# Kernel tuning notes

Measured on AMD Instinct MI355X. Metric: run time of the kernel, lower is better.

Reference implementation:

```python
import jax, jax.numpy as jnp
import numpy as np

V, D, DK, H, HID, NB = 8192, 768, 64, 12, 3072, 4
B, S = 4, 1024


def setup_inputs() -> dict:
    key = jax.random.key(0)
    ks = jax.random.split(key, 10)
    def n(k, shape):
        return jax.random.normal(k, shape, jnp.float32) * 0.02
    return dict(
        X=jax.random.uniform(ks[0], (B, S, V), jnp.float32),
        emb_w=n(ks[1], (V, D)), emb_b=jnp.zeros((D,), jnp.float32),
        Wq=n(ks[2], (NB, H, D, DK)), bq=jnp.zeros((NB, H, DK), jnp.float32),
        Wk=n(ks[3], (NB, H, D, DK)), bk=jnp.zeros((NB, H, DK), jnp.float32),
        Wv=n(ks[4], (NB, H, D, DK)), bv=jnp.zeros((NB, H, DK), jnp.float32),
        Wo=n(ks[5], (NB, H * DK, D)), bo=jnp.zeros((NB, D), jnp.float32),
        W1=n(ks[6], (NB, D, HID)), b1=jnp.zeros((NB, HID), jnp.float32),
        W2=n(ks[7], (NB, HID, D)), b2=jnp.zeros((NB, D), jnp.float32),
        Wout=n(ks[8], (D, V)), bout=jnp.zeros((V,), jnp.float32),
    )


def layernorm(X):
    # custom LayerNorm: no eps, no affine, population variance over dim 2
    mu = jnp.mean(X, axis=2, keepdims=True)
    sigma = jnp.sqrt(jnp.mean(jnp.square(X - mu), axis=2, keepdims=True))
    return (X - mu) / sigma


def reference(X, emb_w, emb_b, Wq, bq, Wk, bk, Wv, bv, Wo, bo, W1, b1, W2, b2, Wout, bout):
    b, s, _ = X.shape
    sqrt_dk = jnp.sqrt(jnp.float32(DK))
    causal = jnp.tril(jnp.ones((s, s), bool))  # tril applied to scores BEFORE softmax (zeros, not -inf) — faithful
    X = X @ emb_w + emb_b  # [b,s,d]
    for i in range(NB):
        Q = jnp.einsum('bsd,hde->bhse', X, Wq[i]) + bq[i][None, :, None, :]
        K = jnp.einsum('bsd,hde->bhse', X, Wk[i]) + bk[i][None, :, None, :]
        Vv = jnp.einsum('bsd,hde->bhse', X, Wv[i]) + bv[i][None, :, None, :]
        scores = jnp.einsum('bhqe,bhke->bhqk', Q, K)
        scores = jnp.where(causal, scores, 0.0) / sqrt_dk
        A = jax.nn.softmax(scores, axis=-1)
        # original einsum 'ijk,ijl->ijl': sum attention weights over k, scale V
        head_out = jnp.sum(A, axis=-1, keepdims=True) * Vv  # [b,h,s,dk]
        cat = head_out.transpose(0, 2, 1, 3).reshape(b, s, H * DK)
        O = cat @ Wo[i] + bo[i]
        X = layernorm(X + O)
        F = jax.nn.relu(X @ W1[i] + b1[i]) @ W2[i] + b2[i]
        X = layernorm(X + F)
    return jax.nn.softmax(X @ Wout + bout, axis=2)
```

## Files before the change

### kernel.cpp

```cpp
#include <hip/hip_runtime.h>

typedef __bf16 bf16_t;
typedef __bf16 bf16x8 __attribute__((ext_vector_type(8)));
typedef float f32x4 __attribute__((ext_vector_type(4)));

#define BM 128
#define BN 128
#define BK 32
#define LDK 40

__device__ inline uint4 pack_bf16x8(float4 a, float4 b)
{
    union { bf16_t h[8]; uint4 u; } cv;
    cv.h[0] = (bf16_t)a.x; cv.h[1] = (bf16_t)a.y;
    cv.h[2] = (bf16_t)a.z; cv.h[3] = (bf16_t)a.w;
    cv.h[4] = (bf16_t)b.x; cv.h[5] = (bf16_t)b.y;
    cv.h[6] = (bf16_t)b.z; cv.h[7] = (bf16_t)b.w;
    return cv.u;
}

template<bool AF32>
__global__ __launch_bounds__(256, 2)
void gemm_bf16(const bf16_t* __restrict__ A, const float* __restrict__ Af,
               const bf16_t* __restrict__ Bt, const float* __restrict__ bias,
               float* __restrict__ Cf, bf16_t* __restrict__ Cbf,
               int M, int N, int K, int relu, int kChunk, long zStride)
{
    __shared__ bf16_t As[BM * LDK];
    __shared__ bf16_t Bs[BN * LDK];

    const int tid  = threadIdx.x;
    const int m0   = blockIdx.y * BM;
    const int n0   = blockIdx.x * BN;
    const int z    = blockIdx.z;
    const int wave = tid >> 6;
    const int lane = tid & 63;
    const int wm   = (wave & 1) * 64;
    const int wn   = (wave >> 1) * 64;
    const int lr   = lane & 15;
    const int lq   = lane >> 4;

    int kBeg = 0, kEnd = K;
    const float* biasP = bias;
    if (kChunk > 0) {
        kBeg = z * kChunk;
        kEnd = min(K, kBeg + kChunk);
        Cf  += (long)z * M * N;
        if (z != 0) biasP = nullptr;
    } else if (zStride != 0) {
        if constexpr (AF32) Af += (long)z * zStride;
        else                A  += (long)z * zStride;
        Bt += (long)z * zStride;
        if (Cf)  Cf  += (long)z * zStride;
        if (Cbf) Cbf += (long)z * zStride;
    }

    f32x4 acc[4][4];
#pragma unroll
    for (int i = 0; i < 4; i++)
#pragma unroll
        for (int j = 0; j < 4; j++) acc[i][j] = (f32x4){0.f, 0.f, 0.f, 0.f};

    const int c0 = tid, c1 = tid + 256;
    const int ar0 = c0 >> 2, ak0 = (c0 & 3) * 8;
    const int ar1 = c1 >> 2, ak1 = (c1 & 3) * 8;

    const bf16_t* Bptr = Bt + (long)n0 * K;

    for (int k0 = kBeg; k0 < kEnd; k0 += BK) {
        uint4 av0, av1;
        if constexpr (AF32) {
            const float* p0 = Af + (long)(m0 + ar0) * K + k0 + ak0;
            const float* p1 = Af + (long)(m0 + ar1) * K + k0 + ak1;
            float4 a00 = *(const float4*)p0, a01 = *(const float4*)(p0 + 4);
            float4 a10 = *(const float4*)p1, a11 = *(const float4*)(p1 + 4);
            av0 = pack_bf16x8(a00, a01);
            av1 = pack_bf16x8(a10, a11);
        } else {
            av0 = *(const uint4*)(A + (long)(m0 + ar0) * K + k0 + ak0);
            av1 = *(const uint4*)(A + (long)(m0 + ar1) * K + k0 + ak1);
        }
        uint4 bv0 = *(const uint4*)(Bptr + (long)ar0 * K + k0 + ak0);
        uint4 bv1 = *(const uint4*)(Bptr + (long)ar1 * K + k0 + ak1);
        __syncthreads();
        *(uint4*)&As[ar0 * LDK + ak0] = av0;
        *(uint4*)&As[ar1 * LDK + ak1] = av1;
        *(uint4*)&Bs[ar0 * LDK + ak0] = bv0;
        *(uint4*)&Bs[ar1 * LDK + ak1] = bv1;
        __syncthreads();

        bf16x8 af[4], bfr[4];
#pragma unroll
        for (int i = 0; i < 4; i++) {
            af[i]  = *(bf16x8*)&As[(wm + i * 16 + lr) * LDK + lq * 8];
            bfr[i] = *(bf16x8*)&Bs[(wn + i * 16 + lr) * LDK + lq * 8];
        }
#pragma unroll
        for (int i = 0; i < 4; i++)
#pragma unroll
            for (int j = 0; j < 4; j++)
                acc[i][j] = __builtin_amdgcn_mfma_f32_16x16x32_bf16(
                    af[i], bfr[j], acc[i][j], 0, 0, 0);
    }

#pragma unroll
    for (int i = 0; i < 4; i++) {
#pragma unroll
        for (int j = 0; j < 4; j++) {
            const int col = n0 + wn + j * 16 + lr;
            const float bval = biasP ? biasP[col] : 0.f;
#pragma unroll
            for (int r = 0; r < 4; r++) {
                const int row = m0 + wm + i * 16 + lq * 4 + r;
                float v = acc[i][j][r] + bval;
                if (relu) v = fmaxf(v, 0.f);
                const long idx = (long)row * N + col;
                if (Cf)  Cf[idx] = v;
                if (Cbf) Cbf[idx] = (bf16_t)v;
            }
        }
    }
}

__global__ void transpose_cast(const float* __restrict__ in, bf16_t* __restrict__ out,
                               int R, int C, long inStrideZ, long outStrideZ)
{
    __shared__ float t[32][33];
    const float* inz = in + inStrideZ * blockIdx.z;
    bf16_t* outz = out + outStrideZ * blockIdx.z;
    const int c0 = blockIdx.x * 32;
    const int r0 = blockIdx.y * 32;
    const int tx = threadIdx.x, ty = threadIdx.y;
#pragma unroll
    for (int dy = 0; dy < 32; dy += 8)
        t[ty + dy][tx] = inz[(long)(r0 + ty + dy) * C + c0 + tx];
    __syncthreads();
#pragma unroll
    for (int dy = 0; dy < 32; dy += 8)
        outz[(long)(c0 + ty + dy) * R + r0 + tx] = (bf16_t)t[tx][ty + dy];
}

__global__ void build_wvn(const float* __restrict__ Wv, bf16_t* __restrict__ WvN)
{
    const long o = (long)blockIdx.x * 256 + threadIdx.x;
    const int e = (int)(o & 63);
    const int h = (int)((o >> 6) % 12);
    const long t = o / 768;
    const int d = (int)(t % 768);
    const int i = (int)(t / 768);
    WvN[o] = (bf16_t)Wv[(((long)(i * 12 + h) * 768 + d) << 6) + e];
}

__global__ __launch_bounds__(256)
void build_bvo(const float* __restrict__ Wo, const float* __restrict__ bv,
               const float* __restrict__ bo, float* __restrict__ bvo)
{
    const int i = blockIdx.y;
    const int j = blockIdx.x * 256 + threadIdx.x;
    const float* w = Wo + (long)i * 589824 + j;
    const float* b = bv + i * 768;
    float s = bo[i * 768 + j];
    for (int n = 0; n < 768; n++) s += b[n] * w[(long)n * 768];
    bvo[i * 768 + j] = s;
}

__global__ __launch_bounds__(256)
void reduce_cast(const float* __restrict__ P, long pStride, int nP,
                 float* __restrict__ outF, bf16_t* __restrict__ outBf, long n)
{
    const long i = ((long)blockIdx.x * 256 + threadIdx.x) * 4;
    if (i >= n) return;
    float4 s = *(const float4*)(P + i);
    for (int p = 1; p < nP; p++) {
        float4 t = *(const float4*)(P + (long)p * pStride + i);
        s.x += t.x; s.y += t.y; s.z += t.z; s.w += t.w;
    }
    *(float4*)(outF + i) = s;
    union { bf16_t h[4]; uint2 u; } cv;
    cv.h[0] = (bf16_t)s.x; cv.h[1] = (bf16_t)s.y;
    cv.h[2] = (bf16_t)s.z; cv.h[3] = (bf16_t)s.w;
    *(uint2*)(outBf + i) = cv.u;
}

__global__ __launch_bounds__(256)
void ln_residual(float* __restrict__ X, const float* __restrict__ P,
                 long pStride, int nP, bf16_t* __restrict__ Xbf)
{
    __shared__ float red[8];
    const long base = (long)blockIdx.x * 768;
    const int tid = threadIdx.x;
    float s[3];
#pragma unroll
    for (int j = 0; j < 3; j++) {
        const int idx = tid + j * 256;
        float v = X[base + idx];
        for (int p = 0; p < nP; p++) v += P[(long)p * pStride + base + idx];
        s[j] = v;
    }
    float sum = s[0] + s[1] + s[2];
    for (int o = 32; o > 0; o >>= 1) sum += __shfl_down(sum, o, 64);
    if ((tid & 63) == 0) red[tid >> 6] = sum;
    __syncthreads();
    const float mu = (red[0] + red[1] + red[2] + red[3]) * (1.0f / 768.0f);
    float d0 = s[0] - mu, d1 = s[1] - mu, d2 = s[2] - mu;
    float sq = d0 * d0 + d1 * d1 + d2 * d2;
    for (int o = 32; o > 0; o >>= 1) sq += __shfl_down(sq, o, 64);
    if ((tid & 63) == 0) red[4 + (tid >> 6)] = sq;
    __syncthreads();
    const float var = (red[4] + red[5] + red[6] + red[7]) * (1.0f / 768.0f);
    const float rstd = 1.0f / sqrtf(var);
#pragma unroll
    for (int j = 0; j < 3; j++) {
        const int idx = tid + j * 256;
        const float v = (s[j] - mu) * rstd;
        X[base + idx] = v;
        Xbf[base + idx] = (bf16_t)v;
    }
}

__global__ __launch_bounds__(256)
void softmax_inplace(float* __restrict__ P)
{
    __shared__ float red[8];
    const long base = (long)blockIdx.x * 8192;
    const int tid = threadIdx.x;
    float v[32];
    float mx = -1e30f;
#pragma unroll
    for (int j = 0; j < 32; j++) {
        v[j] = P[base + tid + j * 256];
        mx = fmaxf(mx, v[j]);
    }
    for (int o = 32; o > 0; o >>= 1) mx = fmaxf(mx, __shfl_down(mx, o, 64));
    if ((tid & 63) == 0) red[tid >> 6] = mx;
    __syncthreads();
    mx = fmaxf(fmaxf(red[0], red[1]), fmaxf(red[2], red[3]));
    float sum = 0.f;
#pragma unroll
    for (int j = 0; j < 32; j++) {
        v[j] = __expf(v[j] - mx);
        sum += v[j];
    }
    for (int o = 32; o > 0; o >>= 1) sum += __shfl_down(sum, o, 64);
    if ((tid & 63) == 0) red[4 + (tid >> 6)] = sum;
    __syncthreads();
    const float inv = 1.0f / (red[4] + red[5] + red[6] + red[7]);
#pragma unroll
    for (int j = 0; j < 32; j++) P[base + tid + j * 256] = v[j] * inv;
}

extern "C" void kernel_launch(void* const* d_in, const int* in_sizes, int n_in,
                              void* d_out, int out_size, void* d_ws, size_t ws_size,
                              hipStream_t stream)
{
    (void)in_sizes; (void)n_in; (void)out_size; (void)ws_size;
    const float* X0   = (const float*)d_in[0];
    const float* embw = (const float*)d_in[1];
    const float* embb = (const float*)d_in[2];
    const float* Wv   = (const float*)d_in[7];
    const float* bv   = (const float*)d_in[8];
    const float* Wo   = (const float*)d_in[9];
    const float* bo   = (const float*)d_in[10];
    const float* W1   = (const float*)d_in[11];
    const float* b1   = (const float*)d_in[12];
    const float* W2   = (const float*)d_in[13];
    const float* b2   = (const float*)d_in[14];
    const float* Wout = (const float*)d_in[15];
    const float* bout = (const float*)d_in[16];
    float* out = (float*)d_out;

    char* base = (char*)d_ws;
    float*  P     = (float*)base;
    bf16_t* WvN   = (bf16_t*)base;
    bf16_t* WoT   = (bf16_t*)(base + 4718592);
    bf16_t* WoutT = (bf16_t*)base;
    bf16_t* Hid   = (bf16_t*)(base + 50331648);
    bf16_t* embT  = (bf16_t*)(base + 75497472);
    bf16_t* WvoT  = (bf16_t*)(base + 88080384);
    float*  bvo   = (float*)(base + 92798976);
    bf16_t* W1T   = (bf16_t*)(base + 92811264);
    bf16_t* W2T   = (bf16_t*)(base + 111685632);
    float*  Xf    = (float*)(base + 130560000);
    bf16_t* Xbf   = (bf16_t*)(base + 143142912);

    const dim3 tb(32, 8);
    const long MN = 3145728;

    transpose_cast<<<dim3(24, 256, 1), tb, 0, stream>>>(embw, embT, 8192, 768, 0, 0);
    transpose_cast<<<dim3(24, 24, 4), tb, 0, stream>>>(Wo, WoT, 768, 768, 589824, 589824);
    build_wvn<<<9216, 256, 0, stream>>>(Wv, WvN);
    build_bvo<<<dim3(3, 4), 256, 0, stream>>>(Wo, bv, bo, bvo);
    gemm_bf16<false><<<dim3(6, 6, 4), 256, 0, stream>>>(
        WoT, nullptr, WvN, nullptr, nullptr, WvoT, 768, 768, 768, 0, 0, 589824L);
    transpose_cast<<<dim3(96, 24, 4), tb, 0, stream>>>(W1, W1T, 768, 3072, 2359296, 2359296);
    transpose_cast<<<dim3(24, 96, 4), tb, 0, stream>>>(W2, W2T, 3072, 768, 2359296, 2359296);

    gemm_bf16<true><<<dim3(6, 32, 4), 256, 0, stream>>>(
        nullptr, X0, embT, embb, P, nullptr, 4096, 768, 8192, 0, 2048, 0);
    reduce_cast<<<3072, 256, 0, stream>>>(P, MN, 4, Xf, Xbf, MN);

    for (int i = 0; i < 4; i++) {
        gemm_bf16<false><<<dim3(6, 32, 2), 256, 0, stream>>>(
            Xbf, nullptr, WvoT + (size_t)i * 589824, bvo + i * 768, P, nullptr,
            4096, 768, 768, 0, 384, 0);
        ln_residual<<<4096, 256, 0, stream>>>(Xf, P, MN, 2, Xbf);
        gemm_bf16<false><<<dim3(24, 32), 256, 0, stream>>>(
            Xbf, nullptr, W1T + (size_t)i * 2359296, b1 + i * 3072, nullptr, Hid,
            4096, 3072, 768, 1, 0, 0);
        gemm_bf16<false><<<dim3(6, 32, 4), 256, 0, stream>>>(
            Hid, nullptr, W2T + (size_t)i * 2359296, b2 + i * 768, P, nullptr,
            4096, 768, 3072, 0, 768, 0);
        ln_residual<<<4096, 256, 0, stream>>>(Xf, P, MN, 4, Xbf);
    }

    transpose_cast<<<dim3(256, 24, 1), tb, 0, stream>>>(Wout, WoutT, 768, 8192, 0, 0);
    gemm_bf16<false><<<dim3(64, 32), 256, 0, stream>>>(
        Xbf, nullptr, WoutT, bout, out, nullptr, 4096, 8192, 768, 0, 0, 0);
    softmax_inplace<<<4096, 256, 0, stream>>>(out);
}
```

Baseline: 1.143 ms.

## Store split-K partials and logits in bf16, remap GEMM block order, vectorize LN

Split-K partial sums and final logits are now written as bf16 instead of fp32, which halves partial-buffer traffic; the reductions, LayerNorm and softmax read the bf16 data and convert it back. The GEMM block index is remapped so groups of eight blocks share an N tile, which is meant to improve L2 reuse. Split-K factors change (embedding 4→8, attention-output 2→4), and LayerNorm uses 192 threads with vectorized loads. Rounding partials and logits to bf16 costs accuracy, and the higher split counts add extra partial buffers to reduce.

```diff
diff --git a/kernel.cpp b/kernel.cpp
--- a/kernel.cpp
+++ b/kernel.cpp
@@ -1,6 +1,7 @@
 #include <hip/hip_runtime.h>
 
 typedef __bf16 bf16_t;
+typedef __bf16 bf16x4 __attribute__((ext_vector_type(4)));
 typedef __bf16 bf16x8 __attribute__((ext_vector_type(8)));
 typedef float f32x4 __attribute__((ext_vector_type(4)));
 
@@ -29,10 +30,19 @@
     __shared__ bf16_t As[BM * LDK];
     __shared__ bf16_t Bs[BN * LDK];
 
+    const int gx = gridDim.x, gy = gridDim.y;
+    const long L = blockIdx.x + (long)gx * (blockIdx.y + (long)gy * blockIdx.z);
+    const int  r = (int)(L & 7);
+    const long t = L >> 3;
+    const int  bx = (int)(t % gx);
+    const long g  = r + 8 * (t / gx);
+    const int  by = (int)(g % gy);
+    const int  bz = (int)(g / gy);
+
     const int tid  = threadIdx.x;
-    const int m0   = blockIdx.y * BM;
-    const int n0   = blockIdx.x * BN;
-    const int z    = blockIdx.z;
+    const int m0   = by * BM;
+    const int n0   = bx * BN;
+    const int z    = bz;
     const int wave = tid >> 6;
     const int lane = tid & 63;
     const int wm   = (wave & 1) * 64;
@@ -45,7 +55,8 @@
     if (kChunk > 0) {
         kBeg = z * kChunk;
         kEnd = min(K, kBeg + kChunk);
-        Cf  += (long)z * M * N;
+        if (Cbf) Cbf += (long)z * M * N;
+        else     Cf  += (long)z * M * N;
         if (z != 0) biasP = nullptr;
     } else if (zStride != 0) {
         if constexpr (AF32) Af += (long)z * zStride;
@@ -110,9 +121,9 @@
             const int col = n0 + wn + j * 16 + lr;
             const float bval = biasP ? biasP[col] : 0.f;
 #pragma unroll
-            for (int r = 0; r < 4; r++) {
-                const int row = m0 + wm + i * 16 + lq * 4 + r;
-                float v = acc[i][j][r] + bval;
+            for (int rr = 0; rr < 4; rr++) {
+                const int row = m0 + wm + i * 16 + lq * 4 + rr;
+                float v = acc[i][j][rr] + bval;
                 if (relu) v = fmaxf(v, 0.f);
                 const long idx = (long)row * N + col;
                 if (Cf)  Cf[idx] = v;
@@ -165,61 +176,64 @@
 }
 
 __global__ __launch_bounds__(256)
-void reduce_cast(const float* __restrict__ P, long pStride, int nP,
+void reduce_cast(const bf16_t* __restrict__ P, long pStride, int nP,
                  float* __restrict__ outF, bf16_t* __restrict__ outBf, long n)
 {
-    const long i = ((long)blockIdx.x * 256 + threadIdx.x) * 4;
-    if (i >= n) return;
-    float4 s = *(const float4*)(P + i);
-    for (int p = 1; p < nP; p++) {
-        float4 t = *(const float4*)(P + (long)p * pStride + i);
-        s.x += t.x; s.y += t.y; s.z += t.z; s.w += t.w;
-    }
-    *(float4*)(outF + i) = s;
-    union { bf16_t h[4]; uint2 u; } cv;
-    cv.h[0] = (bf16_t)s.x; cv.h[1] = (bf16_t)s.y;
-    cv.h[2] = (bf16_t)s.z; cv.h[3] = (bf16_t)s.w;
-    *(uint2*)(outBf + i) = cv.u;
-}
-
-__global__ __launch_bounds__(256)
-void ln_residual(float* __restrict__ X, const float* __restrict__ P,
+    const long i = ((long)blockIdx.x * 256 + threadIdx.x) * 8;
+    if (i + 8 > n) return;
+    float s[8] = {0.f, 0.f, 0.f, 0.f, 0.f, 0.f, 0.f, 0.f};
+    for (int p = 0; p < nP; p++) {
+        bf16x8 v = *(const bf16x8*)(P + (long)p * pStride + i);
+#pragma unroll
+        for (int e = 0; e < 8; e++) s[e] += (float)v[e];
+    }
+    *(float4*)(outF + i)     = (float4){s[0], s[1], s[2], s[3]};
+    *(float4*)(outF + i + 4) = (float4){s[4], s[5], s[6], s[7]};
+    union { bf16_t h[8]; uint4 u; } cv;
+#pragma unroll
+    for (int e = 0; e < 8; e++) cv.h[e] = (bf16_t)s[e];
+    *(uint4*)(outBf + i) = cv.u;
+}
+
+__global__ __launch_bounds__(192)
+void ln_residual(float* __restrict__ X, const bf16_t* __restrict__ P,
                  long pStride, int nP, bf16_t* __restrict__ Xbf)
 {
     __shared__ float red[8];
     const long base = (long)blockIdx.x * 768;
     const int tid = threadIdx.x;
-    float s[3];
-#pragma unroll
-    for (int j = 0; j < 3; j++) {
-        const int idx = tid + j * 256;
-        float v = X[base + idx];
-        for (int p = 0; p < nP; p++) v += P[(long)p * pStride + base + idx];
-        s[j] = v;
-    }
-    float sum = s[0] + s[1] + s[2];
+    const int i0 = tid * 4;
+    float4 xv = *(const float4*)(X + base + i0);
+    float s[4] = {xv.x, xv.y, xv.z, xv.w};
+    for (int p = 0; p < nP; p++) {
+        bf16x4 pv = *(const bf16x4*)(P + (long)p * pStride + base + i0);
+        s[0] += (float)pv[0]; s[1] += (float)pv[1];
+        s[2] += (float)pv[2]; s[3] += (float)pv[3];
+    }
+    float sum = s[0] + s[1] + s[2] + s[3];
     for (int o = 32; o > 0; o >>= 1) sum += __shfl_down(sum, o, 64);
     if ((tid & 63) == 0) red[tid >> 6] = sum;
     __syncthreads();
-    const float mu = (red[0] + red[1] + red[2] + red[3]) * (1.0f / 768.0f);
-    float d0 = s[0] - mu, d1 = s[1] - mu, d2 = s[2] - mu;
-    float sq = d0 * d0 + d1 * d1 + d2 * d2;
+    const float mu = (red[0] + red[1] + red[2]) * (1.0f / 768.0f);
+    float d0 = s[0] - mu, d1 = s[1] - mu, d2 = s[2] - mu, d3 = s[3] - mu;
+    float sq = d0 * d0 + d1 * d1 + d2 * d2 + d3 * d3;
     for (int o = 32; o > 0; o >>= 1) sq += __shfl_down(sq, o, 64);
     if ((tid & 63) == 0) red[4 + (tid >> 6)] = sq;
     __syncthreads();
-    const float var = (red[4] + red[5] + red[6] + red[7]) * (1.0f / 768.0f);
+    const float var = (red[4] + red[5] + red[6]) * (1.0f / 768.0f);
     const float rstd = 1.0f / sqrtf(var);
-#pragma unroll
-    for (int j = 0; j < 3; j++) {
-        const int idx = tid + j * 256;
+    union { bf16_t h[4]; uint2 u; } cv;
+#pragma unroll
+    for (int j = 0; j < 4; j++) {
         const float v = (s[j] - mu) * rstd;
-        X[base + idx] = v;
-        Xbf[base + idx] = (bf16_t)v;
-    }
+        X[base + i0 + j] = v;
+        cv.h[j] = (bf16_t)v;
+    }
+    *(uint2*)(Xbf + base + i0) = cv.u;
 }
 
 __global__ __launch_bounds__(256)
-void softmax_inplace(float* __restrict__ P)
+void softmax_bf16(const bf16_t* __restrict__ L, float* __restrict__ out)
 {
     __shared__ float red[8];
     const long base = (long)blockIdx.x * 8192;
@@ -227,9 +241,13 @@
     float v[32];
     float mx = -1e30f;
 #pragma unroll
-    for (int j = 0; j < 32; j++) {
-        v[j] = P[base + tid + j * 256];
-        mx = fmaxf(mx, v[j]);
+    for (int gq = 0; gq < 4; gq++) {
+        bf16x8 h = *(const bf16x8*)(L + base + gq * 2048 + tid * 8);
+#pragma unroll
+        for (int e = 0; e < 8; e++) {
+            v[gq * 8 + e] = (float)h[e];
+            mx = fmaxf(mx, v[gq * 8 + e]);
+        }
     }
     for (int o = 32; o > 0; o >>= 1) mx = fmaxf(mx, __shfl_down(mx, o, 64));
     if ((tid & 63) == 0) red[tid >> 6] = mx;
@@ -246,7 +264,13 @@
     __syncthreads();
     const float inv = 1.0f / (red[4] + red[5] + red[6] + red[7]);
 #pragma unroll
-    for (int j = 0; j < 32; j++) P[base + tid + j * 256] = v[j] * inv;
+    for (int gq = 0; gq < 4; gq++) {
+        const long o0 = base + gq * 2048 + tid * 8;
+        *(float4*)(out + o0) = (float4){v[gq*8+0]*inv, v[gq*8+1]*inv,
+                                        v[gq*8+2]*inv, v[gq*8+3]*inv};
+        *(float4*)(out + o0 + 4) = (float4){v[gq*8+4]*inv, v[gq*8+5]*inv,
+                                            v[gq*8+6]*inv, v[gq*8+7]*inv};
+    }
 }
 
 extern "C" void kernel_launch(void* const* d_in, const int* in_sizes, int n_in,
@@ -270,12 +294,13 @@
     float* out = (float*)d_out;
 
     char* base = (char*)d_ws;
-    float*  P     = (float*)base;
+    bf16_t* P     = (bf16_t*)base;
     bf16_t* WvN   = (bf16_t*)base;
     bf16_t* WoT   = (bf16_t*)(base + 4718592);
-    bf16_t* WoutT = (bf16_t*)base;
+    bf16_t* Lbf   = (bf16_t*)base;
     bf16_t* Hid   = (bf16_t*)(base + 50331648);
     bf16_t* embT  = (bf16_t*)(base + 75497472);
+    bf16_t* WoutT = (bf16_t*)(base + 75497472);
     bf16_t* WvoT  = (bf16_t*)(base + 88080384);
     float*  bvo   = (float*)(base + 92798976);
     bf16_t* W1T   = (bf16_t*)(base + 92811264);
@@ -295,26 +320,26 @@
     transpose_cast<<<dim3(96, 24, 4), tb, 0, stream>>>(W1, W1T, 768, 3072, 2359296, 2359296);
     transpose_cast<<<dim3(24, 96, 4), tb, 0, stream>>>(W2, W2T, 3072, 768, 2359296, 2359296);
 
-    gemm_bf16<true><<<dim3(6, 32, 4), 256, 0, stream>>>(
-        nullptr, X0, embT, embb, P, nullptr, 4096, 768, 8192, 0, 2048, 0);
-    reduce_cast<<<3072, 256, 0, stream>>>(P, MN, 4, Xf, Xbf, MN);
+    gemm_bf16<true><<<dim3(6, 32, 8), 256, 0, stream>>>(
+        nullptr, X0, embT, embb, nullptr, P, 4096, 768, 8192, 0, 1024, 0);
+    reduce_cast<<<1536, 256, 0, stream>>>(P, MN, 8, Xf, Xbf, MN);
 
     for (int i = 0; i < 4; i++) {
-        gemm_bf16<false><<<dim3(6, 32, 2), 256, 0, stream>>>(
-            Xbf, nullptr, WvoT + (size_t)i * 589824, bvo + i * 768, P, nullptr,
-            4096, 768, 768, 0, 384, 0);
-        ln_residual<<<4096, 256, 0, stream>>>(Xf, P, MN, 2, Xbf);
+        gemm_bf16<false><<<dim3(6, 32, 4), 256, 0, stream>>>(
+            Xbf, nullptr, WvoT + (size_t)i * 589824, bvo + i * 768, nullptr, P,
+            4096, 768, 768, 0, 192, 0);
+        ln_residual<<<4096, 192, 0, stream>>>(Xf, P, MN, 4, Xbf);
         gemm_bf16<false><<<dim3(24, 32), 256, 0, stream>>>(
             Xbf, nullptr, W1T + (size_t)i * 2359296, b1 + i * 3072, nullptr, Hid,
             4096, 3072, 768, 1, 0, 0);
         gemm_bf16<false><<<dim3(6, 32, 4), 256, 0, stream>>>(
-            Hid, nullptr, W2T + (size_t)i * 2359296, b2 + i * 768, P, nullptr,
+            Hid, nullptr, W2T + (size_t)i * 2359296, b2 + i * 768, nullptr, P,
             4096, 768, 3072, 0, 768, 0);
-        ln_residual<<<4096, 256, 0, stream>>>(Xf, P, MN, 4, Xbf);
+        ln_residual<<<4096, 192, 0, stream>>>(Xf, P, MN, 4, Xbf);
     }
 
     transpose_cast<<<dim3(256, 24, 1), tb, 0, stream>>>(Wout, WoutT, 768, 8192, 0, 0);
     gemm_bf16<false><<<dim3(64, 32), 256, 0, stream>>>(
-        Xbf, nullptr, WoutT, bout, out, nullptr, 4096, 8192, 768, 0, 0, 0);
-    softmax_inplace<<<4096, 256, 0, stream>>>(out);
-}
+        Xbf, nullptr, WoutT, bout, nullptr, Lbf, 4096, 8192, 768, 0, 0, 0);
+    softmax_bf16<<<4096, 256, 0, stream>>>(Lbf, out);
+}
```

New measurement: 1.087 ms. 1.05x faster.
